# Kernel tuning notes

Measured on AMD Instinct MI355X. Metric: run time of the kernel, lower is better.

The kernel has to match this reference:

```python
import jax, jax.numpy as jnp
import numpy as np

B, T, I, H = 256, 512, 64, 256  # batch, seq_len, NUM_BANDS, HIDDEN_DIM; NUM_LAYERS=2


def setup_inputs() -> dict:
    key = jax.random.key(0)
    ks = jax.random.split(key, 12)
    s = 0.05
    f = jnp.float32
    return {
        "x": jax.random.normal(ks[0], (B, T, I), f),
        # layer 0 (input -> hidden)
        "W_ih0": jax.random.normal(ks[1], (H, I), f) * s,
        "W_hh0": jax.random.normal(ks[2], (H, H), f) * s,
        "b_ih0": jax.random.normal(ks[3], (H,), f) * s,
        "b_hh0": jax.random.normal(ks[4], (H,), f) * s,
        # layer 1 (hidden -> hidden)
        "W_ih1": jax.random.normal(ks[5], (H, H), f) * s,
        "W_hh1": jax.random.normal(ks[6], (H, H), f) * s,
        "b_ih1": jax.random.normal(ks[7], (H,), f) * s,
        "b_hh1": jax.random.normal(ks[8], (H,), f) * s,
        # fc head (hidden -> 1)
        "W_fc": jax.random.normal(ks[9], (1, H), f) * s,
        "b_fc": jax.random.normal(ks[10], (1,), f) * s,
    }


def _rnn_layer(x_seq, W_ih, W_hh, b_ih, b_hh):
    """Elman ReLU layer: h_t = relu(W_ih x_t + b_ih + W_hh h_{t-1} + b_hh).
    x_seq: [B, T, D] -> returns [B, T, H]. Input projection is batched; only
    the hidden recurrence runs in the scan."""
    pre = jnp.einsum('btd,hd->bth', x_seq, W_ih) + b_ih + b_hh  # [B,T,H]
    h0 = jnp.zeros((x_seq.shape[0], W_hh.shape[0]), x_seq.dtype)

    def step(h, p_t):
        h = jax.nn.relu(p_t + h @ W_hh.T)
        return h, h

    _, ys = jax.lax.scan(step, h0, jnp.swapaxes(pre, 0, 1))  # [T,B,H]
    return jnp.swapaxes(ys, 0, 1)


def reference(x, W_ih0, W_hh0, b_ih0, b_hh0, W_ih1, W_hh1, b_ih1, b_hh1, W_fc, b_fc):
    h1 = _rnn_layer(x, W_ih0, W_hh0, b_ih0, b_hh0)
    h2 = _rnn_layer(h1, W_ih1, W_hh1, b_ih1, b_hh1)
    out = h2.reshape(-1, h2.shape[-1]) @ W_fc.T + b_fc  # [B*T, 1]
    return out.reshape(-1)
```

## Files before the change

kernel.cpp:

```cpp
#include <hip/hip_runtime.h>


#define B_ 256
#define T_ 512
#define I_ 64
#define H_ 256

#define PIN4(v) asm volatile("" : "+v"((v).x), "+v"((v).y), "+v"((v).z), "+v"((v).w))

__device__ __forceinline__ float red8(float a) {
    a += __shfl_xor(a, 1, 64);
    a += __shfl_xor(a, 2, 64);
    a += __shfl_xor(a, 4, 64);
    return a;
}

__global__ __launch_bounds__(512, 1) void k_layer0(
    const float* __restrict__ x, const float* __restrict__ Wih,
    const float* __restrict__ Whh, const float* __restrict__ bih,
    const float* __restrict__ bhh, float* __restrict__ h1out)
{
    const int tid = threadIdx.x;
    const int s = tid & 7;
    const int g = tid >> 3;
    const int b = blockIdx.x;

    float4 whh[4][8], wih[4][2];
#pragma unroll
    for (int r = 0; r < 4; ++r) {
        const float4* pw = (const float4*)(Whh + (size_t)(4 * g + r) * H_ + 32 * s);
#pragma unroll
        for (int i = 0; i < 8; ++i) whh[r][i] = pw[i];
        const float4* px = (const float4*)(Wih + (size_t)(4 * g + r) * I_ + 8 * s);
        wih[r][0] = px[0]; wih[r][1] = px[1];
    }
#pragma unroll
    for (int r = 0; r < 4; ++r) {
#pragma unroll
        for (int i = 0; i < 8; ++i) PIN4(whh[r][i]);
        PIN4(wih[r][0]); PIN4(wih[r][1]);
    }
    float4 bias4;
    {
        float4 b1 = ((const float4*)bih)[g], b2 = ((const float4*)bhh)[g];
        bias4 = make_float4(b1.x + b2.x, b1.y + b2.y, b1.z + b2.z, b1.w + b2.w);
    }

    __shared__ float4 hbuf[2][72];
    __shared__ float4 xs[(32 * I_) / 4];

    if (tid < 64) hbuf[0][tid + (tid >> 3)] = make_float4(0.f, 0.f, 0.f, 0.f);
    const int wloc = g + (g >> 3);

    int p = 0;
#pragma unroll 1
    for (int t0 = 0; t0 < T_; t0 += 32) {
        xs[tid] = ((const float4*)(x + ((size_t)b * T_ + t0) * I_))[tid];
        __syncthreads();
#pragma unroll 1
        for (int tt = 0; tt < 32; ++tt) {
            float4 hv[8];
            const float4* hp = &hbuf[p][9 * s];
#pragma unroll
            for (int i = 0; i < 8; ++i) hv[i] = hp[i];
            float4 xv0, xv1;
            {
                const float4* xp = xs + tt * (I_ / 4) + 2 * s;
                xv0 = xp[0]; xv1 = xp[1];
            }
            float a[4] = {0.f, 0.f, 0.f, 0.f};
#pragma unroll
            for (int r = 0; r < 4; ++r) {
#pragma unroll
                for (int i = 0; i < 8; ++i) {
                    a[r] = fmaf(hv[i].x, whh[r][i].x, a[r]);
                    a[r] = fmaf(hv[i].y, whh[r][i].y, a[r]);
                    a[r] = fmaf(hv[i].z, whh[r][i].z, a[r]);
                    a[r] = fmaf(hv[i].w, whh[r][i].w, a[r]);
                }
                a[r] = fmaf(xv0.x, wih[r][0].x, a[r]);
                a[r] = fmaf(xv0.y, wih[r][0].y, a[r]);
                a[r] = fmaf(xv0.z, wih[r][0].z, a[r]);
                a[r] = fmaf(xv0.w, wih[r][0].w, a[r]);
                a[r] = fmaf(xv1.x, wih[r][1].x, a[r]);
                a[r] = fmaf(xv1.y, wih[r][1].y, a[r]);
                a[r] = fmaf(xv1.z, wih[r][1].z, a[r]);
                a[r] = fmaf(xv1.w, wih[r][1].w, a[r]);
            }
#pragma unroll
            for (int r = 0; r < 4; ++r) a[r] = red8(a[r]);
            float4 v;
            v.x = fmaxf(a[0] + bias4.x, 0.f);
            v.y = fmaxf(a[1] + bias4.y, 0.f);
            v.z = fmaxf(a[2] + bias4.z, 0.f);
            v.w = fmaxf(a[3] + bias4.w, 0.f);
            if (s == 0) {
                hbuf[p ^ 1][wloc] = v;
                ((float4*)(h1out + ((size_t)b * T_ + t0 + tt) * H_))[g] = v;
            }
            __syncthreads();
            p ^= 1;
        }
    }
}

__global__ __launch_bounds__(512, 1) void k_inproj1(
    float* __restrict__ buf, const float* __restrict__ Wih,
    const float* __restrict__ bih, const float* __restrict__ bhh)
{
    const int tid = threadIdx.x;
    const int s = tid & 7, g = tid >> 3;

    float4 w[4][8];
#pragma unroll
    for (int r = 0; r < 4; ++r) {
        const float4* pw = (const float4*)(Wih + (size_t)(4 * g + r) * H_ + 32 * s);
#pragma unroll
        for (int i = 0; i < 8; ++i) w[r][i] = pw[i];
    }
#pragma unroll
    for (int r = 0; r < 4; ++r)
#pragma unroll
        for (int i = 0; i < 8; ++i) PIN4(w[r][i]);
    float4 bias4;
    {
        float4 b1 = ((const float4*)bih)[g], b2 = ((const float4*)bhh)[g];
        bias4 = make_float4(b1.x + b2.x, b1.y + b2.y, b1.z + b2.z, b1.w + b2.w);
    }

    __shared__ float4 rows4[16 * 72];

    const size_t m0 = (size_t)blockIdx.x * 64;
#pragma unroll 1
    for (int c = 0; c < 4; ++c) {
        float* rowbase = buf + (m0 + 16 * c) * H_;
#pragma unroll
        for (int k = 0; k < 4; ++k) {
            const int flat = tid + 512 * k;
            const int r = flat >> 6, e = flat & 63;
            rows4[r * 72 + e + (e >> 3)] = ((const float4*)rowbase)[flat];
        }
        __syncthreads();
#pragma unroll 1
        for (int r = 0; r < 16; ++r) {
            float4 hv[8];
            const float4* hp = &rows4[r * 72 + 9 * s];
#pragma unroll
            for (int i = 0; i < 8; ++i) hv[i] = hp[i];
            float a[4] = {0.f, 0.f, 0.f, 0.f};
#pragma unroll
            for (int q = 0; q < 4; ++q)
#pragma unroll
                for (int i = 0; i < 8; ++i) {
                    a[q] = fmaf(hv[i].x, w[q][i].x, a[q]);
                    a[q] = fmaf(hv[i].y, w[q][i].y, a[q]);
                    a[q] = fmaf(hv[i].z, w[q][i].z, a[q]);
                    a[q] = fmaf(hv[i].w, w[q][i].w, a[q]);
                }
#pragma unroll
            for (int q = 0; q < 4; ++q) a[q] = red8(a[q]);
            if (s == 0) {
                float4 v = make_float4(a[0] + bias4.x, a[1] + bias4.y,
                                       a[2] + bias4.z, a[3] + bias4.w);
                ((float4*)rowbase)[r * (H_ / 4) + g] = v;
            }
        }
        __syncthreads();
    }
}

__global__ __launch_bounds__(512, 1) void k_layer1(
    const float* __restrict__ pre1, const float* __restrict__ Whh,
    const float* __restrict__ Wfc, const float* __restrict__ bfcp,
    float* __restrict__ out)
{
    const int tid = threadIdx.x;
    const int s = tid & 7, g = tid >> 3;
    const int b = blockIdx.x;

    float4 whh[4][8];
#pragma unroll
    for (int r = 0; r < 4; ++r) {
        const float4* pw = (const float4*)(Whh + (size_t)(4 * g + r) * H_ + 32 * s);
#pragma unroll
        for (int i = 0; i < 8; ++i) whh[r][i] = pw[i];
    }
#pragma unroll
    for (int r = 0; r < 4; ++r)
#pragma unroll
        for (int i = 0; i < 8; ++i) PIN4(whh[r][i]);
    const float4 wfc4 = ((const float4*)Wfc)[g];
    const float  bfc  = bfcp[0];

    __shared__ float4 hbuf[2][72];
    __shared__ float4 pchunk[(16 * H_) / 4];
    __shared__ float  wavesum[2][8];

    if (tid < 64) hbuf[0][tid + (tid >> 3)] = make_float4(0.f, 0.f, 0.f, 0.f);
    const int wloc = g + (g >> 3);

    int p = 0;
#pragma unroll 1
    for (int t0 = 0; t0 < T_; t0 += 16) {
        const float4* src = (const float4*)(pre1 + ((size_t)b * T_ + t0) * H_);
        pchunk[tid]       = src[tid];
        pchunk[tid + 512] = src[tid + 512];
        __syncthreads();
#pragma unroll 1
        for (int tt = 0; tt < 16; ++tt) {
            const int t = t0 + tt;
            if (tid == 0 && t > 0) {
                float sfc = bfc;
#pragma unroll
                for (int wv = 0; wv < 8; ++wv) sfc += wavesum[p ^ 1][wv];
                out[(size_t)b * T_ + (t - 1)] = sfc;
            }
            float4 hv[8];
            const float4* hp = &hbuf[p][9 * s];
#pragma unroll
            for (int i = 0; i < 8; ++i) hv[i] = hp[i];
            float a[4] = {0.f, 0.f, 0.f, 0.f};
#pragma unroll
            for (int r = 0; r < 4; ++r)
#pragma unroll
                for (int i = 0; i < 8; ++i) {
                    a[r] = fmaf(hv[i].x, whh[r][i].x, a[r]);
                    a[r] = fmaf(hv[i].y, whh[r][i].y, a[r]);
                    a[r] = fmaf(hv[i].z, whh[r][i].z, a[r]);
                    a[r] = fmaf(hv[i].w, whh[r][i].w, a[r]);
                }
#pragma unroll
            for (int r = 0; r < 4; ++r) a[r] = red8(a[r]);
            const float4 pre = pchunk[tt * (H_ / 4) + g];
            float4 v;
            v.x = fmaxf(a[0] + pre.x, 0.f);
            v.y = fmaxf(a[1] + pre.y, 0.f);
            v.z = fmaxf(a[2] + pre.z, 0.f);
            v.w = fmaxf(a[3] + pre.w, 0.f);
            float fc = v.x * wfc4.x;
            fc = fmaf(v.y, wfc4.y, fc);
            fc = fmaf(v.z, wfc4.z, fc);
            fc = fmaf(v.w, wfc4.w, fc);
            fc += __shfl_xor(fc, 8, 64);
            fc += __shfl_xor(fc, 16, 64);
            fc += __shfl_xor(fc, 32, 64);
            if (s == 0) hbuf[p ^ 1][wloc] = v;
            if ((tid & 63) == 0) wavesum[p][tid >> 6] = fc;
            __syncthreads();
            p ^= 1;
        }
    }
    if (tid == 0) {
        float sfc = bfc;
#pragma unroll
        for (int wv = 0; wv < 8; ++wv) sfc += wavesum[p ^ 1][wv];
        out[(size_t)b * T_ + (T_ - 1)] = sfc;
    }
}

extern "C" void kernel_launch(void* const* d_in, const int* in_sizes, int n_in,
                              void* d_out, int out_size, void* d_ws, size_t ws_size,
                              hipStream_t stream) {
    (void)in_sizes; (void)n_in; (void)out_size; (void)ws_size;
    const float* x    = (const float*)d_in[0];
    const float* Wih0 = (const float*)d_in[1];
    const float* Whh0 = (const float*)d_in[2];
    const float* bih0 = (const float*)d_in[3];
    const float* bhh0 = (const float*)d_in[4];
    const float* Wih1 = (const float*)d_in[5];
    const float* Whh1 = (const float*)d_in[6];
    const float* bih1 = (const float*)d_in[7];
    const float* bhh1 = (const float*)d_in[8];
    const float* Wfc  = (const float*)d_in[9];
    const float* bfc  = (const float*)d_in[10];

    float* buf = (float*)d_ws;
    float* out = (float*)d_out;

    k_layer0 <<<dim3(B_),             dim3(512), 0, stream>>>(x, Wih0, Whh0, bih0, bhh0, buf);
    k_inproj1<<<dim3((B_ * T_) / 64), dim3(512), 0, stream>>>(buf, Wih1, bih1, bhh1);
    k_layer1 <<<dim3(B_),             dim3(512), 0, stream>>>(buf, Whh1, Wfc, bfc, out);
}
```

Before: 1.337 ms.

## Double threads per block to 1024 with 16-way split dot products

All three kernels now launch 1024 threads per block, and each output group is split across 16 lanes instead of 8. Each thread holds half as many weight registers and does half the FMAs per step, with one extra shuffle stage in the reduction. This shortens the serial per-timestep critical path of the recurrence. In exchange the per-step barrier now spans 16 waves instead of 8, and the register-pinning asm is dropped.

```diff
diff --git a/kernel.cpp b/kernel.cpp
--- a/kernel.cpp
+++ b/kernel.cpp
@@ -6,39 +6,39 @@
 #define I_ 64
 #define H_ 256
 
-#define PIN4(v) asm volatile("" : "+v"((v).x), "+v"((v).y), "+v"((v).z), "+v"((v).w))
-
-__device__ __forceinline__ float red8(float a) {
+__device__ __forceinline__ float red16(float a) {
     a += __shfl_xor(a, 1, 64);
     a += __shfl_xor(a, 2, 64);
     a += __shfl_xor(a, 4, 64);
+    a += __shfl_xor(a, 8, 64);
     return a;
 }
 
-__global__ __launch_bounds__(512, 1) void k_layer0(
+#define FMA4(acc, hv, wv)                      \
+    do {                                       \
+        acc = fmaf((hv).x, (wv).x, acc);       \
+        acc = fmaf((hv).y, (wv).y, acc);       \
+        acc = fmaf((hv).z, (wv).z, acc);       \
+        acc = fmaf((hv).w, (wv).w, acc);       \
+    } while (0)
+
+__global__ __launch_bounds__(1024) void k_layer0(
     const float* __restrict__ x, const float* __restrict__ Wih,
     const float* __restrict__ Whh, const float* __restrict__ bih,
     const float* __restrict__ bhh, float* __restrict__ h1out)
 {
     const int tid = threadIdx.x;
-    const int s = tid & 7;
-    const int g = tid >> 3;
+    const int s = tid & 15;
+    const int g = tid >> 4;
     const int b = blockIdx.x;
 
-    float4 whh[4][8], wih[4][2];
+    float4 whh[4][4], wih[4];
 #pragma unroll
     for (int r = 0; r < 4; ++r) {
-        const float4* pw = (const float4*)(Whh + (size_t)(4 * g + r) * H_ + 32 * s);
-#pragma unroll
-        for (int i = 0; i < 8; ++i) whh[r][i] = pw[i];
-        const float4* px = (const float4*)(Wih + (size_t)(4 * g + r) * I_ + 8 * s);
-        wih[r][0] = px[0]; wih[r][1] = px[1];
-    }
-#pragma unroll
-    for (int r = 0; r < 4; ++r) {
-#pragma unroll
-        for (int i = 0; i < 8; ++i) PIN4(whh[r][i]);
-        PIN4(wih[r][0]); PIN4(wih[r][1]);
+        const float4* pw = (const float4*)(Whh + (size_t)(4 * g + r) * H_ + 16 * s);
+#pragma unroll
+        for (int i = 0; i < 4; ++i) whh[r][i] = pw[i];
+        wih[r] = *(const float4*)(Wih + (size_t)(4 * g + r) * I_ + 4 * s);
     }
     float4 bias4;
     {
@@ -55,40 +55,30 @@
     int p = 0;
 #pragma unroll 1
     for (int t0 = 0; t0 < T_; t0 += 32) {
-        xs[tid] = ((const float4*)(x + ((size_t)b * T_ + t0) * I_))[tid];
+        if (tid < 512)
+            xs[tid] = ((const float4*)(x + ((size_t)b * T_ + t0) * I_))[tid];
         __syncthreads();
 #pragma unroll 1
         for (int tt = 0; tt < 32; ++tt) {
-            float4 hv[8];
-            const float4* hp = &hbuf[p][9 * s];
-#pragma unroll
-            for (int i = 0; i < 8; ++i) hv[i] = hp[i];
-            float4 xv0, xv1;
+            float4 hv[4];
             {
-                const float4* xp = xs + tt * (I_ / 4) + 2 * s;
-                xv0 = xp[0]; xv1 = xp[1];
-            }
+                const int e0 = 4 * s;
+#pragma unroll
+                for (int i = 0; i < 4; ++i) {
+                    const int e = e0 + i;
+                    hv[i] = hbuf[p][e + (e >> 3)];
+                }
+            }
+            const float4 xv = xs[tt * (I_ / 4) + s];
             float a[4] = {0.f, 0.f, 0.f, 0.f};
 #pragma unroll
             for (int r = 0; r < 4; ++r) {
 #pragma unroll
-                for (int i = 0; i < 8; ++i) {
-                    a[r] = fmaf(hv[i].x, whh[r][i].x, a[r]);
-                    a[r] = fmaf(hv[i].y, whh[r][i].y, a[r]);
-                    a[r] = fmaf(hv[i].z, whh[r][i].z, a[r]);
-                    a[r] = fmaf(hv[i].w, whh[r][i].w, a[r]);
-                }
-                a[r] = fmaf(xv0.x, wih[r][0].x, a[r]);
-                a[r] = fmaf(xv0.y, wih[r][0].y, a[r]);
-                a[r] = fmaf(xv0.z, wih[r][0].z, a[r]);
-                a[r] = fmaf(xv0.w, wih[r][0].w, a[r]);
-                a[r] = fmaf(xv1.x, wih[r][1].x, a[r]);
-                a[r] = fmaf(xv1.y, wih[r][1].y, a[r]);
-                a[r] = fmaf(xv1.z, wih[r][1].z, a[r]);
-                a[r] = fmaf(xv1.w, wih[r][1].w, a[r]);
-            }
-#pragma unroll
-            for (int r = 0; r < 4; ++r) a[r] = red8(a[r]);
+                for (int i = 0; i < 4; ++i) FMA4(a[r], hv[i], whh[r][i]);
+                FMA4(a[r], xv, wih[r]);
+            }
+#pragma unroll
+            for (int r = 0; r < 4; ++r) a[r] = red16(a[r]);
             float4 v;
             v.x = fmaxf(a[0] + bias4.x, 0.f);
             v.y = fmaxf(a[1] + bias4.y, 0.f);
@@ -104,24 +94,20 @@
     }
 }
 
-__global__ __launch_bounds__(512, 1) void k_inproj1(
+__global__ __launch_bounds__(1024) void k_inproj1(
     float* __restrict__ buf, const float* __restrict__ Wih,
     const float* __restrict__ bih, const float* __restrict__ bhh)
 {
     const int tid = threadIdx.x;
-    const int s = tid & 7, g = tid >> 3;
-
-    float4 w[4][8];
+    const int s = tid & 15, g = tid >> 4;
+
+    float4 w[4][4];
 #pragma unroll
     for (int r = 0; r < 4; ++r) {
-        const float4* pw = (const float4*)(Wih + (size_t)(4 * g + r) * H_ + 32 * s);
-#pragma unroll
-        for (int i = 0; i < 8; ++i) w[r][i] = pw[i];
-    }
-#pragma unroll
-    for (int r = 0; r < 4; ++r)
-#pragma unroll
-        for (int i = 0; i < 8; ++i) PIN4(w[r][i]);
+        const float4* pw = (const float4*)(Wih + (size_t)(4 * g + r) * H_ + 16 * s);
+#pragma unroll
+        for (int i = 0; i < 4; ++i) w[r][i] = pw[i];
+    }
     float4 bias4;
     {
         float4 b1 = ((const float4*)bih)[g], b2 = ((const float4*)bhh)[g];
@@ -134,31 +120,26 @@
 #pragma unroll 1
     for (int c = 0; c < 4; ++c) {
         float* rowbase = buf + (m0 + 16 * c) * H_;
-#pragma unroll
-        for (int k = 0; k < 4; ++k) {
-            const int flat = tid + 512 * k;
-            const int r = flat >> 6, e = flat & 63;
-            rows4[r * 72 + e + (e >> 3)] = ((const float4*)rowbase)[flat];
+        {
+            const int r = tid >> 6, e = tid & 63;
+            rows4[r * 72 + e + (e >> 3)] = ((const float4*)rowbase)[tid];
         }
         __syncthreads();
 #pragma unroll 1
         for (int r = 0; r < 16; ++r) {
-            float4 hv[8];
-            const float4* hp = &rows4[r * 72 + 9 * s];
-#pragma unroll
-            for (int i = 0; i < 8; ++i) hv[i] = hp[i];
+            float4 hv[4];
+#pragma unroll
+            for (int i = 0; i < 4; ++i) {
+                const int e = 4 * s + i;
+                hv[i] = rows4[r * 72 + e + (e >> 3)];
+            }
             float a[4] = {0.f, 0.f, 0.f, 0.f};
 #pragma unroll
             for (int q = 0; q < 4; ++q)
 #pragma unroll
-                for (int i = 0; i < 8; ++i) {
-                    a[q] = fmaf(hv[i].x, w[q][i].x, a[q]);
-                    a[q] = fmaf(hv[i].y, w[q][i].y, a[q]);
-                    a[q] = fmaf(hv[i].z, w[q][i].z, a[q]);
-                    a[q] = fmaf(hv[i].w, w[q][i].w, a[q]);
-                }
-#pragma unroll
-            for (int q = 0; q < 4; ++q) a[q] = red8(a[q]);
+                for (int i = 0; i < 4; ++i) FMA4(a[q], hv[i], w[q][i]);
+#pragma unroll
+            for (int q = 0; q < 4; ++q) a[q] = red16(a[q]);
             if (s == 0) {
                 float4 v = make_float4(a[0] + bias4.x, a[1] + bias4.y,
                                        a[2] + bias4.z, a[3] + bias4.w);
@@ -169,32 +150,28 @@
     }
 }
 
-__global__ __launch_bounds__(512, 1) void k_layer1(
+__global__ __launch_bounds__(1024) void k_layer1(
     const float* __restrict__ pre1, const float* __restrict__ Whh,
     const float* __restrict__ Wfc, const float* __restrict__ bfcp,
     float* __restrict__ out)
 {
     const int tid = threadIdx.x;
-    const int s = tid & 7, g = tid >> 3;
+    const int s = tid & 15, g = tid >> 4;
     const int b = blockIdx.x;
 
-    float4 whh[4][8];
+    float4 whh[4][4];
 #pragma unroll
     for (int r = 0; r < 4; ++r) {
-        const float4* pw = (const float4*)(Whh + (size_t)(4 * g + r) * H_ + 32 * s);
-#pragma unroll
-        for (int i = 0; i < 8; ++i) whh[r][i] = pw[i];
-    }
-#pragma unroll
-    for (int r = 0; r < 4; ++r)
-#pragma unroll
-        for (int i = 0; i < 8; ++i) PIN4(whh[r][i]);
+        const float4* pw = (const float4*)(Whh + (size_t)(4 * g + r) * H_ + 16 * s);
+#pragma unroll
+        for (int i = 0; i < 4; ++i) whh[r][i] = pw[i];
+    }
     const float4 wfc4 = ((const float4*)Wfc)[g];
     const float  bfc  = bfcp[0];
 
     __shared__ float4 hbuf[2][72];
     __shared__ float4 pchunk[(16 * H_) / 4];
-    __shared__ float  wavesum[2][8];
+    __shared__ float  wavesum[2][16];
 
     if (tid < 64) hbuf[0][tid + (tid >> 3)] = make_float4(0.f, 0.f, 0.f, 0.f);
     const int wloc = g + (g >> 3);
@@ -202,9 +179,7 @@
     int p = 0;
 #pragma unroll 1
     for (int t0 = 0; t0 < T_; t0 += 16) {
-        const float4* src = (const float4*)(pre1 + ((size_t)b * T_ + t0) * H_);
-        pchunk[tid]       = src[tid];
-        pchunk[tid + 512] = src[tid + 512];
+        pchunk[tid] = ((const float4*)(pre1 + ((size_t)b * T_ + t0) * H_))[tid];
         __syncthreads();
 #pragma unroll 1
         for (int tt = 0; tt < 16; ++tt) {
@@ -212,25 +187,22 @@
             if (tid == 0 && t > 0) {
                 float sfc = bfc;
 #pragma unroll
-                for (int wv = 0; wv < 8; ++wv) sfc += wavesum[p ^ 1][wv];
+                for (int wv = 0; wv < 16; ++wv) sfc += wavesum[p ^ 1][wv];
                 out[(size_t)b * T_ + (t - 1)] = sfc;
             }
-            float4 hv[8];
-            const float4* hp = &hbuf[p][9 * s];
-#pragma unroll
-            for (int i = 0; i < 8; ++i) hv[i] = hp[i];
+            float4 hv[4];
+#pragma unroll
+            for (int i = 0; i < 4; ++i) {
+                const int e = 4 * s + i;
+                hv[i] = hbuf[p][e + (e >> 3)];
+            }
             float a[4] = {0.f, 0.f, 0.f, 0.f};
 #pragma unroll
             for (int r = 0; r < 4; ++r)
 #pragma unroll
-                for (int i = 0; i < 8; ++i) {
-                    a[r] = fmaf(hv[i].x, whh[r][i].x, a[r]);
-                    a[r] = fmaf(hv[i].y, whh[r][i].y, a[r]);
-                    a[r] = fmaf(hv[i].z, whh[r][i].z, a[r]);
-                    a[r] = fmaf(hv[i].w, whh[r][i].w, a[r]);
-                }
-#pragma unroll
-            for (int r = 0; r < 4; ++r) a[r] = red8(a[r]);
+                for (int i = 0; i < 4; ++i) FMA4(a[r], hv[i], whh[r][i]);
+#pragma unroll
+            for (int r = 0; r < 4; ++r) a[r] = red16(a[r]);
             const float4 pre = pchunk[tt * (H_ / 4) + g];
             float4 v;
             v.x = fmaxf(a[0] + pre.x, 0.f);
@@ -241,7 +213,6 @@
             fc = fmaf(v.y, wfc4.y, fc);
             fc = fmaf(v.z, wfc4.z, fc);
             fc = fmaf(v.w, wfc4.w, fc);
-            fc += __shfl_xor(fc, 8, 64);
             fc += __shfl_xor(fc, 16, 64);
             fc += __shfl_xor(fc, 32, 64);
             if (s == 0) hbuf[p ^ 1][wloc] = v;
@@ -253,7 +224,7 @@
     if (tid == 0) {
         float sfc = bfc;
 #pragma unroll
-        for (int wv = 0; wv < 8; ++wv) sfc += wavesum[p ^ 1][wv];
+        for (int wv = 0; wv < 16; ++wv) sfc += wavesum[p ^ 1][wv];
         out[(size_t)b * T_ + (T_ - 1)] = sfc;
     }
 }
@@ -277,7 +248,7 @@
     float* buf = (float*)d_ws;
     float* out = (float*)d_out;
 
-    k_layer0 <<<dim3(B_),             dim3(512), 0, stream>>>(x, Wih0, Whh0, bih0, bhh0, buf);
-    k_inproj1<<<dim3((B_ * T_) / 64), dim3(512), 0, stream>>>(buf, Wih1, bih1, bhh1);
-    k_layer1 <<<dim3(B_),             dim3(512), 0, stream>>>(buf, Whh1, Wfc, bfc, out);
-}
+    k_layer0 <<<dim3(B_),             dim3(1024), 0, stream>>>(x, Wih0, Whh0, bih0, bhh0, buf);
+    k_inproj1<<<dim3((B_ * T_) / 64), dim3(1024), 0, stream>>>(buf, Wih1, bih1, bhh1);
+    k_layer1 <<<dim3(B_),             dim3(1024), 0, stream>>>(buf, Whh1, Wfc, bfc, out);
+}
```

Measured after the change: 1.741 ms. 30.2% more time.
